# Kernel optimization log

Hardware: AMD Instinct MI355X
Metric: run time of the kernel (lower is better)

Reference implementation:

```python
import jax, jax.numpy as jnp
import numpy as np

THRESHOLD = 0.1


def _conv3x3(x, w, b):
    # x: [B,Ci,H,W], w: [Co,Ci,3,3] -> [B,Co,H,W], SAME padding, ReLU
    y = jax.lax.conv_general_dilated(
        x, w, window_strides=(1, 1), padding='SAME',
        dimension_numbers=('NCHW', 'OIHW', 'NCHW'))
    return jax.nn.relu(y + b[None, :, None, None])


def _autoencoder(x, w1, b1, w2, b2, w3, b3, w4, b4):
    h = _conv3x3(x, w1, b1)          # 64 -> 32
    mid = _conv3x3(h, w2, b2)        # 32 -> 16 (bottleneck)
    h2 = _conv3x3(mid, w3, b3)       # 16 -> 32
    rec = _conv3x3(h2, w4, b4)       # 32 -> 64
    return mid, rec


def setup_inputs() -> dict:
    key = jax.random.key(0)
    ks = jax.random.split(key, 8)
    B, C, H, W = 8, 64, 128, 256
    s = 0.05  # keep activations / singular values at a sane scale
    return {
        'feat0': jax.random.normal(ks[0], (B, C, H, W), jnp.float32),
        'feat1': jax.random.normal(ks[1], (B, C, H, W), jnp.float32),
        'w1': jax.random.normal(ks[2], (32, 64, 3, 3), jnp.float32) * s,
        'b1': jnp.zeros((32,), jnp.float32),
        'w2': jax.random.normal(ks[3], (16, 32, 3, 3), jnp.float32) * s,
        'b2': jnp.zeros((16,), jnp.float32),
        'w3': jax.random.normal(ks[4], (32, 16, 3, 3), jnp.float32) * s,
        'b3': jnp.zeros((32,), jnp.float32),
        'w4': jax.random.normal(ks[5], (64, 32, 3, 3), jnp.float32) * s,
        'b4': jnp.zeros((64,), jnp.float32),
        'modality_adapter': 0,  # accepted but unused by the original forward
    }


def reference(feat0, feat1, w1, b1, w2, b2, w3, b3, w4, b4, modality_adapter):
    feats = [feat0, feat1]
    B, C, H, W = feat0.shape
    auto_enc_loss = jnp.float32(0.0)
    counts_list = []
    for f in feats:
        mid, rec = _autoencoder(f, w1, b1, w2, b2, w3, b3, w4, b4)
        # batched SVD over [B, 16, H*W]; counts of singular values > threshold
        sv = jnp.linalg.svd(jax.lax.stop_gradient(mid.reshape(B, mid.shape[1], H * W)),
                            compute_uv=False)  # [B, 16]
        counts_list.append(jnp.sum(sv > THRESHOLD, axis=1))
        auto_enc_loss = auto_enc_loss + jnp.mean((f - rec) ** 2)
    # pick the dominant modality per batch element
    domain_idx = jnp.argmax(jnp.stack(counts_list, axis=1), axis=1)  # [B]
    con_feat = jnp.stack(feats, axis=1)                              # [B,M,C,H,W]
    dom = con_feat[jnp.arange(B), domain_idx]                        # [B,C,H,W]
    domain_features = jnp.broadcast_to(dom[:, None], con_feat.shape)  # repeat over M
    # two-stage cross-modal einsum attention
    weights = jnp.einsum('smchw,snchw->smnhw', domain_features, con_feat)
    weights = jax.nn.softmax(weights, axis=2)
    weights = jnp.einsum('smnhw,snchw->smchw', weights, con_feat)
    weights = jax.nn.softmax(weights, axis=1)
    fused_feat = jnp.sum(con_feat * weights, axis=1)  # [B,C,H,W]
    return fused_feat, auto_enc_loss
```

## Files before the change

### kernel.cpp

```cpp
#include <hip/hip_runtime.h>
#include <hip/hip_bf16.h>

#define B_ 8
#define H_ 128
#define W_ 256
#define PH 130
#define PW 258
#define NPIX (B_*64*H_*W_)

typedef short short8  __attribute__((ext_vector_type(8)));
typedef short short4v __attribute__((ext_vector_type(4)));
typedef float floatx4 __attribute__((ext_vector_type(4)));

template<int Ci, int Co, bool LOSS, bool NCHW_IN, bool AVG>
__global__ __launch_bounds__(256)
void conv_mfma(const void* __restrict__ inA,
               const void* __restrict__ inB,
               const __hip_bfloat16* __restrict__ wt,
               const float* __restrict__ bias,
               __hip_bfloat16* __restrict__ outp,
               size_t out_mstride,
               const float* __restrict__ ref0,
               const float* __restrict__ ref1,
               const float* __restrict__ other,
               float* __restrict__ avg_out,
               float* __restrict__ acc_out)
{
    constexpr int CC   = (Ci >= 32) ? Ci/32 : 1;
    constexpr int SCI  = NCHW_IN ? 32 : Ci;
    constexpr int PXB  = SCI*2;
    constexpr int NCB  = PXB/16;
    constexpr int SLAB = 6*66*PXB;
    constexpr int NT   = Co/16;
    constexpr int GNT  = (NT >= 2) ? 2 : 1;
    constexpr int NG   = NT / GNT;
    constexpr int EPIW = 64*(Co+8)*2;
    constexpr int RECB = 64*272*2;
    constexpr int LDSZ = LOSS ? (RECB > SLAB ? RECB : SLAB)
                              : (4*EPIW > SLAB ? 4*EPIW : SLAB);
    __shared__ alignas(16) char slab[LDSZ + 32];
    __shared__ float wred[4];

    const int tid  = threadIdx.x;
    const int lane = tid & 63;
    const int wid  = tid >> 6;
    const int col  = lane & 15;
    const int quad = lane >> 4;
    const int w0   = blockIdx.x * 64;
    const int h0   = blockIdx.y * 4;
    const int zz   = blockIdx.z;
    const int bz   = zz & 7;
    const int mz   = zz >> 3;
    const int r    = wid;

    floatx4 acc[4][NT];
#pragma unroll
    for (int mt = 0; mt < 4; ++mt)
#pragma unroll
        for (int nt = 0; nt < NT; ++nt)
            acc[mt][nt] = (floatx4)0.f;

    auto mfma_c2 = [&](int c2) {
#pragma unroll
        for (int g = 0; g < NG; ++g) {
            short8 bfr[9*GNT];
#pragma unroll
            for (int t = 0; t < 9; ++t)
#pragma unroll
                for (int j = 0; j < GNT; ++j)
                    bfr[t*GNT+j] = *(const short8*)(wt
                        + ((size_t)(c2*9+t)*Co + (g*GNT+j)*16 + col)*32 + quad*8);
#pragma unroll
            for (int t = 0; t < 9; ++t) {
                const int dy = t/3, dx = t - (t/3)*3;
                short8 a[4];
#pragma unroll
                for (int mt = 0; mt < 4; ++mt) {
                    int px  = (r+dy)*66 + mt*16 + col + dx;
                    int kch = NCHW_IN ? quad : (c2*4 + quad);
                    a[mt] = *(const short8*)(slab + px*PXB
                              + ((kch ^ (px & (NCB-1))) << 4));
                }
#pragma unroll
                for (int j = 0; j < GNT; ++j)
#pragma unroll
                    for (int mt = 0; mt < 4; ++mt)
                        acc[mt][g*GNT+j] = __builtin_amdgcn_mfma_f32_16x16x32_bf16(
                            a[mt], bfr[t*GNT+j], acc[mt][g*GNT+j], 0, 0, 0);
            }
        }
    };

    if constexpr (NCHW_IN) {
        static_assert(Ci == 64, "NCHW staging is Ci=64 only");
        const float* src = (const float*)(mz ? inB : inA) + (size_t)bz * 64 * H_ * W_;
#pragma unroll
        for (int c2 = 0; c2 < CC; ++c2) {
            if (c2) __syncthreads();
            const float* chb = src + (size_t)(c2*32 + wid*8) * (H_*W_);
#pragma unroll
            for (int it = 0; it < 7; ++it) {
                int pxl = it*64 + lane;
                bool live = (it < 6) || (lane < 12);
                int row = pxl / 66;
                int pxc = pxl - row*66;
                int gh  = h0 + row - 1;
                int gw  = w0 + pxc - 1;
                bool ok = live && ((unsigned)gh < (unsigned)H_)
                               && ((unsigned)gw < (unsigned)W_);
                const float* sp = chb + (size_t)(ok ? gh : 0)*W_ + (ok ? gw : 0);
                short8 v;
#pragma unroll
                for (int j = 0; j < 8; ++j) {
                    float f = sp[(size_t)j*(H_*W_)];
                    v[j] = __builtin_bit_cast(short, __float2bfloat16(ok ? f : 0.f));
                }
                if (live)
                    *(short8*)(slab + pxl*PXB + ((wid ^ (pxl & (NCB-1))) << 4)) = v;
            }
            __syncthreads();
            mfma_c2(c2);
        }
    } else {
        const __hip_bfloat16* inb = (const __hip_bfloat16*)(mz ? inB : inA)
                                    + (size_t)bz * PH * PW * Ci;
        for (int o = tid*16; o < SLAB; o += 4096) {
            int pxl = o / PXB;
            int row = pxl / 66;
            int pxc = pxl - row*66;
            int cb  = (o >> 4) & (NCB-1);
            short8 v = *(const short8*)(inb + ((size_t)(h0+row)*PW + (w0+pxc))*Ci + cb*8);
            *(short8*)(slab + pxl*PXB + ((cb ^ (pxl & (NCB-1))) << 4)) = v;
        }
        __syncthreads();

        if constexpr (Ci >= 32) {
#pragma unroll
            for (int c2 = 0; c2 < CC; ++c2)
                mfma_c2(c2);
        } else {
            short8 bfr[6*NT];
#pragma unroll
            for (int kc = 0; kc < 6; ++kc)
#pragma unroll
                for (int j = 0; j < NT; ++j)
                    bfr[kc*NT+j] = *(const short8*)(wt
                        + ((size_t)kc*Co + j*16 + col)*32 + quad*8);
#pragma unroll
            for (int kc = 0; kc < 6; ++kc) {
                const int dy = kc >> 1, half = kc & 1;
                const int dxe = half ? 2 : (quad >> 1);
                short8 a[4];
#pragma unroll
                for (int mt = 0; mt < 4; ++mt) {
                    int px = (r+dy)*66 + mt*16 + col + dxe;
                    a[mt] = *(const short8*)(slab + px*PXB
                              + (((quad & 1) ^ (px & 1)) << 4));
                }
#pragma unroll
                for (int j = 0; j < NT; ++j)
#pragma unroll
                    for (int mt = 0; mt < 4; ++mt)
                        acc[mt][j] = __builtin_amdgcn_mfma_f32_16x16x32_bf16(
                            a[mt], bfr[kc*NT+j], acc[mt][j], 0, 0, 0);
            }
        }
    }

    if constexpr (!LOSS) {
        __syncthreads();
        char* rt = slab + wid * EPIW;
#pragma unroll
        for (int nt = 0; nt < NT; ++nt) {
            float bv = bias[nt*16 + col];
#pragma unroll
            for (int mt = 0; mt < 4; ++mt) {
#pragma unroll
                for (int rr = 0; rr < 4; ++rr) {
                    float v = acc[mt][nt][rr] + bv;
                    v = v > 0.f ? v : 0.f;
                    int px = mt*16 + quad*4 + rr;
                    *(__hip_bfloat16*)(rt + (px*(Co+8) + nt*16 + col)*2) =
                        __float2bfloat16(v);
                }
            }
        }
        __hip_bfloat16* ob = outp + (size_t)mz * out_mstride;
        char* grow = (char*)ob
            + (((size_t)bz*PH + (h0 + r + 1))*PW + (w0 + 1))*Co*2;
        constexpr int GB = 64*Co*2;
#pragma unroll
        for (int id = 0; id < GB/1024; ++id) {
            int o  = id*1024 + lane*16;
            int px = o / (Co*2);
            int cb = o - px*(Co*2);
            *(short8*)(grow + o) = *(const short8*)(rt + px*(Co+8)*2 + cb);
        }
    } else {
        __syncthreads();
        __hip_bfloat16* rec = (__hip_bfloat16*)slab;
#pragma unroll
        for (int nt = 0; nt < NT; ++nt) {
            int co = nt*16 + col;
            float bv = bias[co];
#pragma unroll
            for (int mt = 0; mt < 4; ++mt) {
                short4v pk;
#pragma unroll
                for (int rr = 0; rr < 4; ++rr) {
                    float v = acc[mt][nt][rr] + bv;
                    v = v > 0.f ? v : 0.f;
                    pk[rr] = __builtin_bit_cast(short, __float2bfloat16(v));
                }
                *(short4v*)(rec + co*272 + r*68 + mt*16 + quad*4) = pk;
            }
        }
        __syncthreads();

        float lsum = 0.f;
        const float* refb = (mz ? ref1 : ref0) + (size_t)bz * 64 * H_ * W_;
#pragma unroll
        for (int i = 0; i < 16; ++i) {
            int row = i & 3, cg = i >> 2;
            int co  = cg*16 + wid*4 + quad;
            size_t off = ((size_t)co*H_ + h0 + row)*W_ + w0 + col*4;
            float4 f = *(const float4*)(refb + off);
            short4v pk = *(const short4v*)(rec + co*272 + row*68 + col*4);
            float d0 = f.x - __bfloat162float(__builtin_bit_cast(__hip_bfloat16, pk[0]));
            float d1 = f.y - __bfloat162float(__builtin_bit_cast(__hip_bfloat16, pk[1]));
            float d2 = f.z - __bfloat162float(__builtin_bit_cast(__hip_bfloat16, pk[2]));
            float d3 = f.w - __bfloat162float(__builtin_bit_cast(__hip_bfloat16, pk[3]));
            lsum += d0*d0 + d1*d1 + d2*d2 + d3*d3;
            if constexpr (AVG) {
                if (mz) {
                    const float* othb = other + (size_t)bz * 64 * H_ * W_;
                    float*       avgb = avg_out + (size_t)bz * 64 * H_ * W_;
                    float4 g = *(const float4*)(othb + off);
                    float4 o;
                    o.x = 0.5f*(f.x + g.x);
                    o.y = 0.5f*(f.y + g.y);
                    o.z = 0.5f*(f.z + g.z);
                    o.w = 0.5f*(f.w + g.w);
                    *(float4*)(avgb + off) = o;
                }
            }
        }
#pragma unroll
        for (int off = 32; off > 0; off >>= 1)
            lsum += __shfl_down(lsum, off, 64);
        if (lane == 0) wred[wid] = lsum;
        __syncthreads();
        if (tid == 0)
            atomicAdd(acc_out, (wred[0] + wred[1] + wred[2] + wred[3])
                               * (1.0f / (float)NPIX));
    }
}

template<int C>
__device__ __forceinline__ void zb_item(__hip_bfloat16* buf, int idx)
{
    constexpr int CP = C/8;
    int cb   = idx % CP;
    int cell = (idx / CP) % 772;
    int img  = idx / (CP*772);
    int row, colp;
    if (cell < 258)      { row = 0;   colp = cell; }
    else if (cell < 516) { row = 129; colp = cell - 258; }
    else { int r2 = cell - 516; row = 1 + (r2 >> 1); colp = (r2 & 1) ? 257 : 0; }
    short8 z = (short8)0;
    *(short8*)(buf + (((size_t)img*PH + row)*PW + colp)*C + cb*8) = z;
}

template<int Ci, int Co>
__device__ __forceinline__ void wt_item(const float* __restrict__ w,
                                        __hip_bfloat16* __restrict__ wt, int idx)
{
    int kl = idx & 31;
    int co = (idx >> 5) % Co;
    int kc = idx / (32*Co);
    float val = 0.f;
    if constexpr (Ci >= 32) {
        int c2 = kc / 9, t = kc % 9;
        int dy = t/3, dx = t%3;
        int ci = c2*32 + kl;
        val = w[((size_t)(co*Ci + ci)*3 + dy)*3 + dx];
    } else {
        int dy = kc >> 1, half = kc & 1;
        int dx = half*2 + (kl >> 4);
        int ci = kl & 15;
        if (dx < 3) val = w[((size_t)(co*Ci + ci)*3 + dy)*3 + dx];
    }
    wt[idx] = __float2bfloat16(val);
}

__global__ __launch_bounds__(256)
void setup_kernel(const float* __restrict__ w1, const float* __restrict__ w2,
                  const float* __restrict__ w3, const float* __restrict__ w4,
                  __hip_bfloat16* WT1, __hip_bfloat16* WT2,
                  __hip_bfloat16* WT3, __hip_bfloat16* WT4,
                  __hip_bfloat16* BUF1, __hip_bfloat16* BUF2,
                  float* acc)
{
    int idx = blockIdx.x*256 + threadIdx.x;
    if (idx == 0) *acc = 0.f;
    if      (idx <  49408) zb_item<32>(BUF1, idx);
    else if (idx <  74112) zb_item<16>(BUF2, idx - 49408);
    else if (idx <  92544) wt_item<64,32>(w1, WT1, idx - 74112);
    else if (idx <  97152) wt_item<32,16>(w2, WT2, idx - 92544);
    else if (idx < 103296) wt_item<16,32>(w3, WT3, idx - 97152);
    else if (idx < 121728) wt_item<32,64>(w4, WT4, idx - 103296);
}

__global__ __launch_bounds__(256)
void fused_avg_kernel(const float4* __restrict__ a, const float4* __restrict__ b,
                      float4* __restrict__ o, int n4)
{
    int i = blockIdx.x*256 + threadIdx.x;
    if (i < n4) {
        float4 x = a[i], y = b[i];
        float4 r;
        r.x = 0.5f*(x.x + y.x);
        r.y = 0.5f*(x.y + y.y);
        r.z = 0.5f*(x.z + y.z);
        r.w = 0.5f*(x.w + y.w);
        o[i] = r;
    }
}

extern "C" void kernel_launch(void* const* d_in, const int* in_sizes, int n_in,
                              void* d_out, int out_size, void* d_ws, size_t ws_size,
                              hipStream_t stream)
{
    const float* feat0 = (const float*)d_in[0];
    const float* feat1 = (const float*)d_in[1];
    const float* w1 = (const float*)d_in[2];
    const float* b1 = (const float*)d_in[3];
    const float* w2 = (const float*)d_in[4];
    const float* b2 = (const float*)d_in[5];
    const float* w3 = (const float*)d_in[6];
    const float* b3 = (const float*)d_in[7];
    const float* w4 = (const float*)d_in[8];
    const float* b4 = (const float*)d_in[9];

    float* out = (float*)d_out;
    float* acc = out + NPIX;

    constexpr size_t B1B = (size_t)B_*PH*PW*32*2;
    constexpr size_t B2B = (size_t)B_*PH*PW*16*2;
    constexpr size_t SCR_SZ = 51612672;
    const bool use_ws = (d_ws != nullptr) && (ws_size >= SCR_SZ);
    char* sb = use_ws ? (char*)d_ws : (char*)d_out;

    __hip_bfloat16* BUF1 = (__hip_bfloat16*)(sb + 0);
    __hip_bfloat16* BUF2 = (__hip_bfloat16*)(sb + 2*B1B);
    __hip_bfloat16* WT1  = (__hip_bfloat16*)(sb + 51517440);
    __hip_bfloat16* WT2  = (__hip_bfloat16*)(sb + 51554304);
    __hip_bfloat16* WT3  = (__hip_bfloat16*)(sb + 51563520);
    __hip_bfloat16* WT4  = (__hip_bfloat16*)(sb + 51575808);

    setup_kernel<<<476, 256, 0, stream>>>(w1, w2, w3, w4,
                                          WT1, WT2, WT3, WT4, BUF1, BUF2, acc);

    dim3 cgrid(W_/64, H_/4, 2*B_);
    dim3 blk(256);

    constexpr size_t B1E = B1B/2;
    constexpr size_t B2E = B2B/2;

    conv_mfma<64,32,false,true ,false><<<cgrid, blk, 0, stream>>>(
        feat0, feat1, WT1, b1, BUF1, B1E,
        nullptr, nullptr, nullptr, nullptr, nullptr);
    conv_mfma<32,16,false,false,false><<<cgrid, blk, 0, stream>>>(
        BUF1, BUF1 + B1E, WT2, b2, BUF2, B2E,
        nullptr, nullptr, nullptr, nullptr, nullptr);
    conv_mfma<16,32,false,false,false><<<cgrid, blk, 0, stream>>>(
        BUF2, BUF2 + B2E, WT3, b3, BUF1, B1E,
        nullptr, nullptr, nullptr, nullptr, nullptr);
    if (use_ws)
        conv_mfma<32,64,true ,false,true ><<<cgrid, blk, 0, stream>>>(
            BUF1, BUF1 + B1E, WT4, b4, nullptr, 0,
            feat0, feat1, feat0, out, acc);
    else {
        conv_mfma<32,64,true ,false,false><<<cgrid, blk, 0, stream>>>(
            BUF1, BUF1 + B1E, WT4, b4, nullptr, 0,
            feat0, feat1, nullptr, nullptr, acc);
        int n4 = NPIX/4;
        fused_avg_kernel<<<(n4 + 255)/256, 256, 0, stream>>>(
            (const float4*)feat0, (const float4*)feat1, (float4*)out, n4);
    }
}
```

Measured before the change: 317.7 us.

## Fuse four conv launches into one persistent kernel with grid barriers

Replaces the four separate conv kernel launches with a single persistent kernel. Its blocks loop over tiles for each conv stage and are separated by atomic-counter grid-wide barriers. The grid is sized from occupancy queries so all blocks are co-resident. The aim is to remove launch gaps and tail effects between stages, at the cost of spin-wait barriers, a fixed LDS size for all stages, and a deadlock risk if the blocks are not all resident.

```diff
diff --git a/kernel.cpp b/kernel.cpp
--- a/kernel.cpp
+++ b/kernel.cpp
@@ -12,9 +12,22 @@
 typedef short short4v __attribute__((ext_vector_type(4)));
 typedef float floatx4 __attribute__((ext_vector_type(4)));
 
+template<int Ci, int Co, bool LOSS, bool NCHW_IN>
+struct conv_cfg {
+    static constexpr int SCI  = NCHW_IN ? 32 : Ci;
+    static constexpr int PXB  = SCI*2;
+    static constexpr int SLAB = 6*66*PXB;
+    static constexpr int EPIW = 64*(Co+8)*2;
+    static constexpr int RECB = 64*272*2;
+    static constexpr int LDSZ = LOSS ? (RECB > SLAB ? RECB : SLAB)
+                                     : (4*EPIW > SLAB ? 4*EPIW : SLAB);
+};
+
 template<int Ci, int Co, bool LOSS, bool NCHW_IN, bool AVG>
-__global__ __launch_bounds__(256)
-void conv_mfma(const void* __restrict__ inA,
+__device__ __forceinline__
+void conv_tile(int tx, int ty, int bz, int mz,
+               char* __restrict__ slab, float* __restrict__ wred,
+               const void* __restrict__ inA,
                const void* __restrict__ inB,
                const __hip_bfloat16* __restrict__ wt,
                const float* __restrict__ bias,
@@ -27,31 +40,24 @@
                float* __restrict__ acc_out)
 {
     constexpr int CC   = (Ci >= 32) ? Ci/32 : 1;
-    constexpr int SCI  = NCHW_IN ? 32 : Ci;
-    constexpr int PXB  = SCI*2;
+    constexpr int PXB  = conv_cfg<Ci,Co,LOSS,NCHW_IN>::PXB;
     constexpr int NCB  = PXB/16;
-    constexpr int SLAB = 6*66*PXB;
+    constexpr int SLAB = conv_cfg<Ci,Co,LOSS,NCHW_IN>::SLAB;
     constexpr int NT   = Co/16;
     constexpr int GNT  = (NT >= 2) ? 2 : 1;
     constexpr int NG   = NT / GNT;
-    constexpr int EPIW = 64*(Co+8)*2;
-    constexpr int RECB = 64*272*2;
-    constexpr int LDSZ = LOSS ? (RECB > SLAB ? RECB : SLAB)
-                              : (4*EPIW > SLAB ? 4*EPIW : SLAB);
-    __shared__ alignas(16) char slab[LDSZ + 32];
-    __shared__ float wred[4];
+    constexpr int EPIW = conv_cfg<Ci,Co,LOSS,NCHW_IN>::EPIW;
 
     const int tid  = threadIdx.x;
     const int lane = tid & 63;
     const int wid  = tid >> 6;
     const int col  = lane & 15;
     const int quad = lane >> 4;
-    const int w0   = blockIdx.x * 64;
-    const int h0   = blockIdx.y * 4;
-    const int zz   = blockIdx.z;
-    const int bz   = zz & 7;
-    const int mz   = zz >> 3;
+    const int w0   = tx * 64;
+    const int h0   = ty * 4;
     const int r    = wid;
+
+    __syncthreads();
 
     floatx4 acc[4][NT];
 #pragma unroll
@@ -256,6 +262,90 @@
     }
 }
 
+__device__ __forceinline__ void grid_sync(int* cnt, int target)
+{
+    __syncthreads();
+    if (threadIdx.x == 0) {
+        __threadfence();
+        __hip_atomic_fetch_add(cnt, 1, __ATOMIC_ACQ_REL, __HIP_MEMORY_SCOPE_AGENT);
+        while (__hip_atomic_load(cnt, __ATOMIC_ACQUIRE, __HIP_MEMORY_SCOPE_AGENT)
+               < target)
+            __builtin_amdgcn_s_sleep(1);
+        __threadfence();
+    }
+    __syncthreads();
+}
+
+__global__ __launch_bounds__(256, 4)
+void fused_chain(const float* __restrict__ feat0, const float* __restrict__ feat1,
+                 const __hip_bfloat16* __restrict__ WT1,
+                 const __hip_bfloat16* __restrict__ WT2,
+                 const __hip_bfloat16* __restrict__ WT3,
+                 const __hip_bfloat16* __restrict__ WT4,
+                 const float* __restrict__ b1, const float* __restrict__ b2,
+                 const float* __restrict__ b3, const float* __restrict__ b4,
+                 __hip_bfloat16* __restrict__ BUF1, __hip_bfloat16* __restrict__ BUF2,
+                 float* __restrict__ avg_out, float* __restrict__ acc,
+                 int* __restrict__ cnt)
+{
+    constexpr int LDSZ = 64*272*2;
+    __shared__ alignas(16) char slab[LDSZ + 32];
+    __shared__ float wred[4];
+    constexpr size_t B1E = (size_t)B_*PH*PW*32;
+    constexpr size_t B2E = (size_t)B_*PH*PW*16;
+    const int gsz = gridDim.x;
+
+    int tx, ty, bz, mz;
+    auto dec = [&](int t) {
+        tx = t & 3; ty = (t >> 2) & 31; bz = (t >> 7) & 7; mz = t >> 10;
+    };
+
+    for (int t = blockIdx.x; t < 2048; t += gsz) {
+        dec(t);
+        conv_tile<64,32,false,true ,false>(tx,ty,bz,mz, slab, wred,
+            feat0, feat1, WT1, b1, BUF1, B1E,
+            nullptr, nullptr, nullptr, nullptr, nullptr);
+    }
+    grid_sync(cnt, 1*gsz);
+    for (int t = blockIdx.x; t < 2048; t += gsz) {
+        dec(t);
+        conv_tile<32,16,false,false,false>(tx,ty,bz,mz, slab, wred,
+            BUF1, BUF1 + B1E, WT2, b2, BUF2, B2E,
+            nullptr, nullptr, nullptr, nullptr, nullptr);
+    }
+    grid_sync(cnt, 2*gsz);
+    for (int t = blockIdx.x; t < 2048; t += gsz) {
+        dec(t);
+        conv_tile<16,32,false,false,false>(tx,ty,bz,mz, slab, wred,
+            BUF2, BUF2 + B2E, WT3, b3, BUF1, B1E,
+            nullptr, nullptr, nullptr, nullptr, nullptr);
+    }
+    grid_sync(cnt, 3*gsz);
+    for (int t = blockIdx.x; t < 2048; t += gsz) {
+        dec(t);
+        conv_tile<32,64,true ,false,true >(tx,ty,bz,mz, slab, wred,
+            BUF1, BUF1 + B1E, WT4, b4, nullptr, 0,
+            feat0, feat1, feat0, avg_out, acc);
+    }
+}
+
+template<int Ci, int Co, bool LOSS, bool NCHW_IN, bool AVG>
+__global__ __launch_bounds__(256)
+void conv_mfma(const void* __restrict__ inA, const void* __restrict__ inB,
+               const __hip_bfloat16* __restrict__ wt, const float* __restrict__ bias,
+               __hip_bfloat16* __restrict__ outp, size_t out_mstride,
+               const float* __restrict__ ref0, const float* __restrict__ ref1,
+               const float* __restrict__ other, float* __restrict__ avg_out,
+               float* __restrict__ acc_out)
+{
+    constexpr int LDSZ = conv_cfg<Ci,Co,LOSS,NCHW_IN>::LDSZ;
+    __shared__ alignas(16) char slab[LDSZ + 32];
+    __shared__ float wred[4];
+    conv_tile<Ci,Co,LOSS,NCHW_IN,AVG>(blockIdx.x, blockIdx.y,
+        blockIdx.z & 7, blockIdx.z >> 3, slab, wred,
+        inA, inB, wt, bias, outp, out_mstride, ref0, ref1, other, avg_out, acc_out);
+}
+
 template<int C>
 __device__ __forceinline__ void zb_item(__hip_bfloat16* buf, int idx)
 {
@@ -299,10 +389,10 @@
                   __hip_bfloat16* WT1, __hip_bfloat16* WT2,
                   __hip_bfloat16* WT3, __hip_bfloat16* WT4,
                   __hip_bfloat16* BUF1, __hip_bfloat16* BUF2,
-                  float* acc)
+                  float* acc, int* cnt)
 {
     int idx = blockIdx.x*256 + threadIdx.x;
-    if (idx == 0) *acc = 0.f;
+    if (idx == 0) { *acc = 0.f; *cnt = 0; }
     if      (idx <  49408) zb_item<32>(BUF1, idx);
     else if (idx <  74112) zb_item<16>(BUF2, idx - 49408);
     else if (idx <  92544) wt_item<64,32>(w1, WT1, idx - 74112);
@@ -346,8 +436,7 @@
     float* acc = out + NPIX;
 
     constexpr size_t B1B = (size_t)B_*PH*PW*32*2;
-    constexpr size_t B2B = (size_t)B_*PH*PW*16*2;
-    constexpr size_t SCR_SZ = 51612672;
+    constexpr size_t SCR_SZ = 51612736;
     const bool use_ws = (d_ws != nullptr) && (ws_size >= SCR_SZ);
     char* sb = use_ws ? (char*)d_ws : (char*)d_out;
 
@@ -357,35 +446,56 @@
     __hip_bfloat16* WT2  = (__hip_bfloat16*)(sb + 51554304);
     __hip_bfloat16* WT3  = (__hip_bfloat16*)(sb + 51563520);
     __hip_bfloat16* WT4  = (__hip_bfloat16*)(sb + 51575808);
+    int*            CNT  = (int*)(sb + 51612672);
 
     setup_kernel<<<476, 256, 0, stream>>>(w1, w2, w3, w4,
-                                          WT1, WT2, WT3, WT4, BUF1, BUF2, acc);
-
-    dim3 cgrid(W_/64, H_/4, 2*B_);
-    dim3 blk(256);
+                                          WT1, WT2, WT3, WT4, BUF1, BUF2, acc, CNT);
+
+    static int g_nblk = 0;
+    if (g_nblk == 0) {
+        int bpc = 0;
+        if (hipOccupancyMaxActiveBlocksPerMultiprocessor(&bpc, fused_chain, 256, 0)
+                != hipSuccess || bpc < 1)
+            bpc = 0;
+        int dev = 0; hipGetDevice(&dev);
+        int ncu = 0;
+        if (hipDeviceGetAttribute(&ncu, hipDeviceAttributeMultiprocessorCount, dev)
+                != hipSuccess || ncu <= 0)
+            ncu = 256;
+        g_nblk = (bpc >= 1) ? bpc * ncu : -1;
+        if (g_nblk > 2048) g_nblk = 2048;
+    }
 
     constexpr size_t B1E = B1B/2;
-    constexpr size_t B2E = B2B/2;
-
-    conv_mfma<64,32,false,true ,false><<<cgrid, blk, 0, stream>>>(
-        feat0, feat1, WT1, b1, BUF1, B1E,
-        nullptr, nullptr, nullptr, nullptr, nullptr);
-    conv_mfma<32,16,false,false,false><<<cgrid, blk, 0, stream>>>(
-        BUF1, BUF1 + B1E, WT2, b2, BUF2, B2E,
-        nullptr, nullptr, nullptr, nullptr, nullptr);
-    conv_mfma<16,32,false,false,false><<<cgrid, blk, 0, stream>>>(
-        BUF2, BUF2 + B2E, WT3, b3, BUF1, B1E,
-        nullptr, nullptr, nullptr, nullptr, nullptr);
-    if (use_ws)
-        conv_mfma<32,64,true ,false,true ><<<cgrid, blk, 0, stream>>>(
-            BUF1, BUF1 + B1E, WT4, b4, nullptr, 0,
-            feat0, feat1, feat0, out, acc);
-    else {
-        conv_mfma<32,64,true ,false,false><<<cgrid, blk, 0, stream>>>(
-            BUF1, BUF1 + B1E, WT4, b4, nullptr, 0,
-            feat0, feat1, nullptr, nullptr, acc);
-        int n4 = NPIX/4;
-        fused_avg_kernel<<<(n4 + 255)/256, 256, 0, stream>>>(
-            (const float4*)feat0, (const float4*)feat1, (float4*)out, n4);
-    }
-}
+    constexpr size_t B2E = (size_t)B_*PH*PW*16;
+
+    if (use_ws && g_nblk > 0) {
+        fused_chain<<<g_nblk, 256, 0, stream>>>(
+            feat0, feat1, WT1, WT2, WT3, WT4, b1, b2, b3, b4,
+            BUF1, BUF2, out, acc, CNT);
+    } else {
+        dim3 cgrid(W_/64, H_/4, 2*B_);
+        dim3 blk(256);
+        conv_mfma<64,32,false,true ,false><<<cgrid, blk, 0, stream>>>(
+            feat0, feat1, WT1, b1, BUF1, B1E,
+            nullptr, nullptr, nullptr, nullptr, nullptr);
+        conv_mfma<32,16,false,false,false><<<cgrid, blk, 0, stream>>>(
+            BUF1, BUF1 + B1E, WT2, b2, BUF2, B2E,
+            nullptr, nullptr, nullptr, nullptr, nullptr);
+        conv_mfma<16,32,false,false,false><<<cgrid, blk, 0, stream>>>(
+            BUF2, BUF2 + B2E, WT3, b3, BUF1, B1E,
+            nullptr, nullptr, nullptr, nullptr, nullptr);
+        if (use_ws)
+            conv_mfma<32,64,true ,false,true ><<<cgrid, blk, 0, stream>>>(
+                BUF1, BUF1 + B1E, WT4, b4, nullptr, 0,
+                feat0, feat1, feat0, out, acc);
+        else {
+            conv_mfma<32,64,true ,false,false><<<cgrid, blk, 0, stream>>>(
+                BUF1, BUF1 + B1E, WT4, b4, nullptr, 0,
+                feat0, feat1, nullptr, nullptr, acc);
+            int n4 = NPIX/4;
+            fused_avg_kernel<<<(n4 + 255)/256, 256, 0, stream>>>(
+                (const float4*)feat0, (const float4*)feat1, (float4*)out, n4);
+        }
+    }
+}
```

After: 839.6 us. 2.64x slower.

## Restructure conv pipeline: fold border zeroing into conv1, pair modalities in conv4

Applied to the files above, without the earlier changes.

The conv body becomes a device function, conv_tile, called by dedicated kernels. Zeroing of the padded buffer borders moves from the setup kernel into conv1, conv1's NCHW staging now loads float2 pairs of pixels, and conv4 runs both modalities in one block with a launch-bounds occupancy hint. GNT for Co=64 is lowered to 1, presumably to reduce register pressure. The aim is fewer wide launches and better load vectorization, at the cost of longer per-block work in conv4 and a possible race: conv1 zeroes BUF1 borders while writing BUF1 interiors, and a mistake there would corrupt the padding.

```diff
diff --git a/kernel.cpp b/kernel.cpp
--- a/kernel.cpp
+++ b/kernel.cpp
@@ -12,9 +12,22 @@
 typedef short short4v __attribute__((ext_vector_type(4)));
 typedef float floatx4 __attribute__((ext_vector_type(4)));
 
+template<int Ci, int Co, bool LOSS, bool NCHW_IN>
+struct conv_cfg {
+    static constexpr int SCI  = NCHW_IN ? 32 : Ci;
+    static constexpr int PXB  = SCI*2;
+    static constexpr int SLAB = 6*66*PXB;
+    static constexpr int EPIW = 64*(Co+8)*2;
+    static constexpr int RECB = 64*272*2;
+    static constexpr int LDSZ = LOSS ? (RECB > SLAB ? RECB : SLAB)
+                                     : (4*EPIW > SLAB ? 4*EPIW : SLAB);
+};
+
 template<int Ci, int Co, bool LOSS, bool NCHW_IN, bool AVG>
-__global__ __launch_bounds__(256)
-void conv_mfma(const void* __restrict__ inA,
+__device__ __forceinline__
+void conv_tile(int tx, int ty, int bz, int mz,
+               char* __restrict__ slab, float* __restrict__ wred,
+               const void* __restrict__ inA,
                const void* __restrict__ inB,
                const __hip_bfloat16* __restrict__ wt,
                const float* __restrict__ bias,
@@ -27,31 +40,24 @@
                float* __restrict__ acc_out)
 {
     constexpr int CC   = (Ci >= 32) ? Ci/32 : 1;
-    constexpr int SCI  = NCHW_IN ? 32 : Ci;
-    constexpr int PXB  = SCI*2;
+    constexpr int PXB  = conv_cfg<Ci,Co,LOSS,NCHW_IN>::PXB;
     constexpr int NCB  = PXB/16;
-    constexpr int SLAB = 6*66*PXB;
+    constexpr int SLAB = conv_cfg<Ci,Co,LOSS,NCHW_IN>::SLAB;
     constexpr int NT   = Co/16;
-    constexpr int GNT  = (NT >= 2) ? 2 : 1;
+    constexpr int GNT  = (Co == 64) ? 1 : ((NT >= 2) ? 2 : 1);
     constexpr int NG   = NT / GNT;
-    constexpr int EPIW = 64*(Co+8)*2;
-    constexpr int RECB = 64*272*2;
-    constexpr int LDSZ = LOSS ? (RECB > SLAB ? RECB : SLAB)
-                              : (4*EPIW > SLAB ? 4*EPIW : SLAB);
-    __shared__ alignas(16) char slab[LDSZ + 32];
-    __shared__ float wred[4];
+    constexpr int EPIW = conv_cfg<Ci,Co,LOSS,NCHW_IN>::EPIW;
 
     const int tid  = threadIdx.x;
     const int lane = tid & 63;
     const int wid  = tid >> 6;
     const int col  = lane & 15;
     const int quad = lane >> 4;
-    const int w0   = blockIdx.x * 64;
-    const int h0   = blockIdx.y * 4;
-    const int zz   = blockIdx.z;
-    const int bz   = zz & 7;
-    const int mz   = zz >> 3;
+    const int w0   = tx * 64;
+    const int h0   = ty * 4;
     const int r    = wid;
+
+    __syncthreads();
 
     floatx4 acc[4][NT];
 #pragma unroll
@@ -99,24 +105,48 @@
             if (c2) __syncthreads();
             const float* chb = src + (size_t)(c2*32 + wid*8) * (H_*W_);
 #pragma unroll
-            for (int it = 0; it < 7; ++it) {
-                int pxl = it*64 + lane;
-                bool live = (it < 6) || (lane < 12);
-                int row = pxl / 66;
-                int pxc = pxl - row*66;
-                int gh  = h0 + row - 1;
-                int gw  = w0 + pxc - 1;
-                bool ok = live && ((unsigned)gh < (unsigned)H_)
-                               && ((unsigned)gw < (unsigned)W_);
-                const float* sp = chb + (size_t)(ok ? gh : 0)*W_ + (ok ? gw : 0);
-                short8 v;
-#pragma unroll
-                for (int j = 0; j < 8; ++j) {
-                    float f = sp[(size_t)j*(H_*W_)];
-                    v[j] = __builtin_bit_cast(short, __float2bfloat16(ok ? f : 0.f));
-                }
-                if (live)
-                    *(short8*)(slab + pxl*PXB + ((wid ^ (pxl & (NCB-1))) << 4)) = v;
+            for (int it = 0; it < 4; ++it) {
+                int uu   = it*64 + lane;
+                bool live = (it < 3) || (lane < 12);
+                int row  = uu / 34;
+                int s    = uu - row*34;
+                int gh   = h0 + row - 1;
+                bool okr = live && ((unsigned)gh < (unsigned)H_);
+                if (s < 32) {
+                    int pxc0 = 1 + 2*s;
+                    int gw   = w0 + pxc0 - 1;
+                    const float* rp = chb + (size_t)(okr ? gh : 0)*W_ + gw;
+                    short8 v0, v1;
+#pragma unroll
+                    for (int j = 0; j < 8; ++j) {
+                        float2 f;
+                        if (okr) f = *(const float2*)(rp + (size_t)j*(H_*W_));
+                        else     { f.x = 0.f; f.y = 0.f; }
+                        v0[j] = __builtin_bit_cast(short, __float2bfloat16(f.x));
+                        v1[j] = __builtin_bit_cast(short, __float2bfloat16(f.y));
+                    }
+                    if (live) {
+                        int pxl = row*66 + pxc0;
+                        *(short8*)(slab + pxl*PXB
+                            + ((wid ^ (pxl & (NCB-1))) << 4)) = v0;
+                        *(short8*)(slab + (pxl+1)*PXB
+                            + ((wid ^ ((pxl+1) & (NCB-1))) << 4)) = v1;
+                    }
+                } else if (live) {
+                    int pxc = (s == 32) ? 0 : 65;
+                    int gw  = w0 + pxc - 1;
+                    bool ok = okr && ((unsigned)gw < (unsigned)W_);
+                    const float* rp = chb + (size_t)(ok ? gh : 0)*W_ + (ok ? gw : 0);
+                    short8 v;
+#pragma unroll
+                    for (int j = 0; j < 8; ++j) {
+                        float f = ok ? rp[(size_t)j*(H_*W_)] : 0.f;
+                        v[j] = __builtin_bit_cast(short, __float2bfloat16(f));
+                    }
+                    int pxl = row*66 + pxc;
+                    *(short8*)(slab + pxl*PXB
+                        + ((wid ^ (pxl & (NCB-1))) << 4)) = v;
+                }
             }
             __syncthreads();
             mfma_c2(c2);
@@ -237,10 +267,10 @@
                     float*       avgb = avg_out + (size_t)bz * 64 * H_ * W_;
                     float4 g = *(const float4*)(othb + off);
                     float4 o;
-                    o.x = 0.5f*(f.x + g.x);
-                    o.y = 0.5f*(f.y + g.y);
-                    o.z = 0.5f*(f.z + g.z);
-                    o.w = 0.5f*(f.w + g.w);
+                    o.x = 0.5f*(g.x + f.x);
+                    o.y = 0.5f*(g.y + f.y);
+                    o.z = 0.5f*(g.z + f.z);
+                    o.w = 0.5f*(g.w + f.w);
                     *(float4*)(avgb + off) = o;
                 }
             }
@@ -269,6 +299,63 @@
     else { int r2 = cell - 516; row = 1 + (r2 >> 1); colp = (r2 & 1) ? 257 : 0; }
     short8 z = (short8)0;
     *(short8*)(buf + (((size_t)img*PH + row)*PW + colp)*C + cb*8) = z;
+}
+
+__global__ __launch_bounds__(256)
+void conv1_kernel(const float* __restrict__ feat0, const float* __restrict__ feat1,
+                  const __hip_bfloat16* __restrict__ WT1, const float* __restrict__ b1,
+                  __hip_bfloat16* __restrict__ BUF1, __hip_bfloat16* __restrict__ BUF2,
+                  size_t b1e)
+{
+    constexpr int LDSZ = conv_cfg<64,32,false,true>::LDSZ;
+    __shared__ alignas(16) char slab[LDSZ + 32];
+    __shared__ float wred[4];
+
+    int gtid = ((blockIdx.z*gridDim.y + blockIdx.y)*gridDim.x + blockIdx.x)*256
+               + threadIdx.x;
+    if      (gtid < 49408) zb_item<32>(BUF1, gtid);
+    else if (gtid < 74112) zb_item<16>(BUF2, gtid - 49408);
+
+    conv_tile<64,32,false,true,false>(blockIdx.x, blockIdx.y,
+        blockIdx.z & 7, blockIdx.z >> 3, slab, wred,
+        feat0, feat1, WT1, b1, BUF1, b1e,
+        nullptr, nullptr, nullptr, nullptr, nullptr);
+}
+
+template<int Ci, int Co>
+__global__ __launch_bounds__(256)
+void conv_mid(const __hip_bfloat16* __restrict__ inA,
+              const __hip_bfloat16* __restrict__ inB,
+              const __hip_bfloat16* __restrict__ wt, const float* __restrict__ bias,
+              __hip_bfloat16* __restrict__ outp, size_t out_mstride)
+{
+    constexpr int LDSZ = conv_cfg<Ci,Co,false,false>::LDSZ;
+    __shared__ alignas(16) char slab[LDSZ + 32];
+    __shared__ float wred[4];
+    conv_tile<Ci,Co,false,false,false>(blockIdx.x, blockIdx.y,
+        blockIdx.z & 7, blockIdx.z >> 3, slab, wred,
+        inA, inB, wt, bias, outp, out_mstride,
+        nullptr, nullptr, nullptr, nullptr, nullptr);
+}
+
+template<bool AVG>
+__global__ __launch_bounds__(256, 3)
+void conv4_loss(const __hip_bfloat16* __restrict__ BUF1, size_t b1e,
+                const __hip_bfloat16* __restrict__ WT4, const float* __restrict__ b4,
+                const float* __restrict__ feat0, const float* __restrict__ feat1,
+                float* __restrict__ avg_out, float* __restrict__ acc)
+{
+    constexpr int LDSZ = conv_cfg<32,64,true,false>::LDSZ;
+    __shared__ alignas(16) char slab[LDSZ + 32];
+    __shared__ float wred[4];
+    const int tx = blockIdx.x, ty = blockIdx.y, bz = blockIdx.z;
+
+    conv_tile<32,64,true,false,false>(tx, ty, bz, 0, slab, wred,
+        BUF1, BUF1 + b1e, WT4, b4, nullptr, 0,
+        feat0, feat1, nullptr, nullptr, acc);
+    conv_tile<32,64,true,false,AVG>(tx, ty, bz, 1, slab, wred,
+        BUF1, BUF1 + b1e, WT4, b4, nullptr, 0,
+        feat0, feat1, feat0, avg_out, acc);
 }
 
 template<int Ci, int Co>
@@ -298,17 +385,14 @@
                   const float* __restrict__ w3, const float* __restrict__ w4,
                   __hip_bfloat16* WT1, __hip_bfloat16* WT2,
                   __hip_bfloat16* WT3, __hip_bfloat16* WT4,
-                  __hip_bfloat16* BUF1, __hip_bfloat16* BUF2,
                   float* acc)
 {
     int idx = blockIdx.x*256 + threadIdx.x;
     if (idx == 0) *acc = 0.f;
-    if      (idx <  49408) zb_item<32>(BUF1, idx);
-    else if (idx <  74112) zb_item<16>(BUF2, idx - 49408);
-    else if (idx <  92544) wt_item<64,32>(w1, WT1, idx - 74112);
-    else if (idx <  97152) wt_item<32,16>(w2, WT2, idx - 92544);
-    else if (idx < 103296) wt_item<16,32>(w3, WT3, idx - 97152);
-    else if (idx < 121728) wt_item<32,64>(w4, WT4, idx - 103296);
+    if      (idx < 18432) wt_item<64,32>(w1, WT1, idx);
+    else if (idx < 23040) wt_item<32,16>(w2, WT2, idx - 18432);
+    else if (idx < 29184) wt_item<16,32>(w3, WT3, idx - 23040);
+    else if (idx < 47616) wt_item<32,64>(w4, WT4, idx - 29184);
 }
 
 __global__ __launch_bounds__(256)
@@ -346,7 +430,6 @@
     float* acc = out + NPIX;
 
     constexpr size_t B1B = (size_t)B_*PH*PW*32*2;
-    constexpr size_t B2B = (size_t)B_*PH*PW*16*2;
     constexpr size_t SCR_SZ = 51612672;
     const bool use_ws = (d_ws != nullptr) && (ws_size >= SCR_SZ);
     char* sb = use_ws ? (char*)d_ws : (char*)d_out;
@@ -358,32 +441,28 @@
     __hip_bfloat16* WT3  = (__hip_bfloat16*)(sb + 51563520);
     __hip_bfloat16* WT4  = (__hip_bfloat16*)(sb + 51575808);
 
-    setup_kernel<<<476, 256, 0, stream>>>(w1, w2, w3, w4,
-                                          WT1, WT2, WT3, WT4, BUF1, BUF2, acc);
+    setup_kernel<<<186, 256, 0, stream>>>(w1, w2, w3, w4,
+                                          WT1, WT2, WT3, WT4, acc);
+
+    constexpr size_t B1E = B1B/2;
+    constexpr size_t B2E = (size_t)B_*PH*PW*16;
 
     dim3 cgrid(W_/64, H_/4, 2*B_);
+    dim3 lgrid(W_/64, H_/4, B_);
     dim3 blk(256);
 
-    constexpr size_t B1E = B1B/2;
-    constexpr size_t B2E = B2B/2;
-
-    conv_mfma<64,32,false,true ,false><<<cgrid, blk, 0, stream>>>(
-        feat0, feat1, WT1, b1, BUF1, B1E,
-        nullptr, nullptr, nullptr, nullptr, nullptr);
-    conv_mfma<32,16,false,false,false><<<cgrid, blk, 0, stream>>>(
-        BUF1, BUF1 + B1E, WT2, b2, BUF2, B2E,
-        nullptr, nullptr, nullptr, nullptr, nullptr);
-    conv_mfma<16,32,false,false,false><<<cgrid, blk, 0, stream>>>(
-        BUF2, BUF2 + B2E, WT3, b3, BUF1, B1E,
-        nullptr, nullptr, nullptr, nullptr, nullptr);
-    if (use_ws)
-        conv_mfma<32,64,true ,false,true ><<<cgrid, blk, 0, stream>>>(
-            BUF1, BUF1 + B1E, WT4, b4, nullptr, 0,
-            feat0, feat1, feat0, out, acc);
-    else {
-        conv_mfma<32,64,true ,false,false><<<cgrid, blk, 0, stream>>>(
-            BUF1, BUF1 + B1E, WT4, b4, nullptr, 0,
-            feat0, feat1, nullptr, nullptr, acc);
+    conv1_kernel<<<cgrid, blk, 0, stream>>>(feat0, feat1, WT1, b1,
+                                            BUF1, BUF2, B1E);
+    conv_mid<32,16><<<cgrid, blk, 0, stream>>>(BUF1, BUF1 + B1E, WT2, b2,
+                                               BUF2, B2E);
+    conv_mid<16,32><<<cgrid, blk, 0, stream>>>(BUF2, BUF2 + B2E, WT3, b3,
+                                               BUF1, B1E);
+    if (use_ws) {
+        conv4_loss<true><<<lgrid, blk, 0, stream>>>(BUF1, B1E, WT4, b4,
+                                                    feat0, feat1, out, acc);
+    } else {
+        conv4_loss<false><<<lgrid, blk, 0, stream>>>(BUF1, B1E, WT4, b4,
+                                                     feat0, feat1, nullptr, acc);
         int n4 = NPIX/4;
         fused_avg_kernel<<<(n4 + 255)/256, 256, 0, stream>>>(
             (const float4*)feat0, (const float4*)feat1, (float4*)out, n4);
```

After: 510.2 us. 60.6% more time.
